# Optimization experiments

Measured on AMD Instinct MI355X. Metric: run time of the kernel, lower is better.

The kernel has to match this reference:

```python
import jax, jax.numpy as jnp
import numpy as np

B, N = 64, 16384
D_WHERE, D_WHAT = 4, 64
MAX_OBJECTS = 512
NEG_PCT = 0.1
NEG_ADDED = int(NEG_PCT * N)          # 1638
K = MAX_OBJECTS + NEG_ADDED           # 2150 objects kept per image (static)
EPS = 1e-3                            # _z_present_eps
PRESENT_THRESH = 0.5                  # deterministic present_fn


def setup_inputs() -> dict:
    key = jax.random.key(0)
    k1, k2, k3, k4, k5, k6 = jax.random.split(key, 6)
    return {
        "z_where": jax.random.normal(k1, (B, N, D_WHERE), dtype=jnp.float32),
        "z_present": jax.random.uniform(k2, (B, N, 1), dtype=jnp.float32),
        "z_what_loc": jax.random.normal(k3, (B, N, D_WHAT), dtype=jnp.float32),
        "z_what_scale": jax.random.uniform(k4, (B, N, D_WHAT), dtype=jnp.float32),
        "z_depth_loc": jax.random.normal(k5, (B, N, 1), dtype=jnp.float32),
        "z_depth_scale": jax.random.uniform(k6, (B, N, 1), dtype=jnp.float32),
    }


def _forward(z_where, z_present, z_what_loc, z_what_scale, z_depth_loc, z_depth_scale):
    # --- reset_non_present ---
    mask = z_present > EPS                                # [B,N,1]
    z_what_loc = jnp.where(mask, z_what_loc, jnp.float32(0.0))
    z_what_scale = jnp.where(mask, z_what_scale, jnp.float32(1.0))
    z_depth_loc = jnp.where(mask, z_depth_loc, jnp.float32(0.0))
    z_depth_scale = jnp.where(mask, z_depth_scale, jnp.float32(1.0))

    # --- sampling fns (deterministic instantiation) ---
    sampled_where = z_where
    sampled_present = (z_present > PRESENT_THRESH).astype(z_present.dtype)  # [B,N,1]
    sampled_what = z_what_loc
    sampled_depth = z_depth_loc

    # --- limit_positive: drop lowest-probability present objects beyond cap ---
    # equivalent to keeping top-MAX_OBJECTS present objects by z_present per row
    p = z_present[..., 0]                                 # [B,N]
    pres = sampled_present[..., 0] > 0                    # [B,N] bool
    score = jnp.where(pres, p, -jnp.inf)
    order = jnp.argsort(-score, axis=1)                   # descending, -inf last
    ranks = jnp.argsort(order, axis=1)                    # rank of each slot
    keep = pres & (ranks < MAX_OBJECTS)                   # [B,N]

    # --- add_negative: mark NEG_ADDED zero slots per row with -1 ---
    # (deterministic stand-in for randperm: take the last NEG_ADDED zero slots)
    zero = ~keep                                          # [B,N]
    zcount = jnp.cumsum(zero.astype(jnp.int32), axis=1)   # [B,N]
    nzeros = zcount[:, -1:]                               # [B,1]
    negative = zero & (zcount > nzeros - NEG_ADDED)
    modified = jnp.where(negative, jnp.float32(-1.0), keep.astype(z_present.dtype))

    # --- filter: gather nonzero slots (exactly K per row) in index order ---
    present_mask = modified != 0                          # [B,N]
    sort_key = jnp.where(present_mask, 0, 1).astype(jnp.int32)
    idx = jnp.argsort(sort_key, axis=1, stable=True)[:, :K]  # [B,K]

    def gather(t):
        return jnp.take_along_axis(t, idx[..., None], axis=1)

    return (
        gather(sampled_where),          # [B,K,4]
        gather(modified[..., None]),    # [B,K,1] values in {-1, 1}
        gather(sampled_what),           # [B,K,64]
        gather(sampled_depth),          # [B,K,1]
    )


def reference(z_where, z_present, z_what_loc, z_what_scale, z_depth_loc, z_depth_scale):
    return _forward(z_where, z_present, z_what_loc, z_what_scale,
                    z_depth_loc, z_depth_scale)
```

## Files before the change

kernel.cpp:

```cpp
#include <hip/hip_runtime.h>
#include <cstdint>

#define NB 64
#define NN 16384
#define DWHERE 4
#define DWHAT 64
#define MAXOBJ 512
#define NEGADD 1638
#define KSEL (MAXOBJ + NEGADD)
#define EPSV 0.001f

__device__ __forceinline__ void scan1024(int* buf, int t) {
  #pragma unroll
  for (int off = 1; off < 1024; off <<= 1) {
    int x = (t >= off) ? buf[t - off] : 0;
    __syncthreads();
    buf[t] += x;
    __syncthreads();
  }
}

__global__ __launch_bounds__(1024) void select_kernel(
    const float* __restrict__ z_present,
    int* __restrict__ ws_idx,
    float* __restrict__ ws_mod)
{
  const int b = blockIdx.x;
  const int t = threadIdx.x;

  __shared__ int hist[4096];
  __shared__ int buf[1024];
  __shared__ int s_B1, s_above1, s_T, s_kTie;

  if (t == 0) { s_B1 = -1; s_above1 = 0; s_T = 0; s_kTie = 0; }

  unsigned int key[16];
  {
    const float4* p4 = (const float4*)(z_present + (size_t)b * NN);
    #pragma unroll
    for (int j = 0; j < 4; ++j) {
      float4 v = p4[t * 4 + j];
      key[4 * j + 0] = (v.x > 0.5f) ? __float_as_uint(v.x) : 0u;
      key[4 * j + 1] = (v.y > 0.5f) ? __float_as_uint(v.y) : 0u;
      key[4 * j + 2] = (v.z > 0.5f) ? __float_as_uint(v.z) : 0u;
      key[4 * j + 3] = (v.w > 0.5f) ? __float_as_uint(v.w) : 0u;
    }
  }

  #pragma unroll
  for (int j = 0; j < 4; ++j) hist[t + 1024 * j] = 0;
  __syncthreads();
  #pragma unroll
  for (int j = 0; j < 16; ++j)
    if (key[j]) atomicAdd(&hist[(key[j] >> 12) - 0x3F000u], 1);
  __syncthreads();

  int h0 = hist[2 * t], h1 = hist[2 * t + 1];
  buf[1023 - t] = h0 + h1;
  __syncthreads();
  scan1024(buf, t);
  int sufP  = buf[1023 - t];
  int sufPn = (t == 1023) ? 0 : buf[1022 - t];
  int presentCount = buf[1023];
  if (presentCount > MAXOBJ) {
    int sufE = sufP;
    int sufO = sufP - h0;
    if (sufE >= MAXOBJ && sufO  < MAXOBJ) { s_B1 = 2 * t;     s_above1 = sufO;  }
    if (sufO >= MAXOBJ && sufPn < MAXOBJ) { s_B1 = 2 * t + 1; s_above1 = sufPn; }
  }
  __syncthreads();

  int B1 = s_B1;
  if (B1 >= 0) {
    unsigned int hi = (unsigned int)B1 + 0x3F000u;
    #pragma unroll
    for (int j = 0; j < 4; ++j) hist[t + 1024 * j] = 0;
    __syncthreads();
    #pragma unroll
    for (int j = 0; j < 16; ++j)
      if (key[j] && ((key[j] >> 12) == hi)) atomicAdd(&hist[key[j] & 0xFFFu], 1);
    __syncthreads();
    int g0 = hist[4 * t], g1 = hist[4 * t + 1], g2 = hist[4 * t + 2], g3 = hist[4 * t + 3];
    buf[1023 - t] = g0 + g1 + g2 + g3;
    __syncthreads();
    scan1024(buf, t);
    int sufQ  = buf[1023 - t];
    int sufQn = (t == 1023) ? 0 : buf[1022 - t];
    int rem = MAXOBJ - s_above1;
    int s0 = sufQ;
    int s1 = s0 - g0;
    int s2 = s1 - g1;
    int s3 = s2 - g2;
    int s4 = sufQn;
    unsigned int baseT = hi << 12;
    if (s0 >= rem && s1 < rem) { s_T = (int)(baseT | (4u * t + 0)); s_kTie = rem - s1; }
    if (s1 >= rem && s2 < rem) { s_T = (int)(baseT | (4u * t + 1)); s_kTie = rem - s2; }
    if (s2 >= rem && s3 < rem) { s_T = (int)(baseT | (4u * t + 2)); s_kTie = rem - s3; }
    if (s3 >= rem && s4 < rem) { s_T = (int)(baseT | (4u * t + 3)); s_kTie = rem - s4; }
  }
  __syncthreads();

  const unsigned int T = (unsigned int)s_T;
  const int kTie = s_kTie;

  int tieCnt = 0;
  if (T) {
    #pragma unroll
    for (int j = 0; j < 16; ++j) tieCnt += (key[j] == T) ? 1 : 0;
  }
  __syncthreads();
  buf[t] = tieCnt;
  __syncthreads();
  scan1024(buf, t);
  int tieBase = buf[t] - tieCnt;

  int keepMask = 0, zc = 0;
  {
    int tr = tieBase;
    #pragma unroll
    for (int j = 0; j < 16; ++j) {
      unsigned int kk = key[j];
      bool kp;
      if (kk > T) kp = true;
      else if (T && kk == T) { kp = (tr < kTie); tr++; }
      else kp = false;
      keepMask |= ((int)kp) << j;
      zc += kp ? 0 : 1;
    }
  }
  __syncthreads();
  buf[t] = zc;
  __syncthreads();
  scan1024(buf, t);
  int zBase = buf[t] - zc;
  int Z = buf[1023];

  int thr = Z - NEGADD; if (thr < 0) thr = 0;
  int keepTotal = NN - Z;
  int KselTot = keepTotal + (Z - thr);
  size_t obase = (size_t)b * KSEL;
  int ze = zBase;
  #pragma unroll
  for (int j = 0; j < 16; ++j) {
    int i = t * 16 + j;
    bool kp = (keepMask >> j) & 1;
    int keepBefore = i - ze;
    int negBefore = ze - thr; if (negBefore < 0) negBefore = 0;
    int selBefore = keepBefore + negBefore;
    if (kp) {
      ws_idx[obase + selBefore] = i;
      ws_mod[obase + selBefore] = 1.0f;
    } else {
      if (ze >= thr) {
        ws_idx[obase + selBefore] = i;
        ws_mod[obase + selBefore] = -1.0f;
      } else if (KselTot < KSEL) {
        int slot2 = KselTot + (i - selBefore);
        if (slot2 < KSEL) { ws_idx[obase + slot2] = i; ws_mod[obase + slot2] = 0.0f; }
      }
      ze++;
    }
  }
}

__global__ __launch_bounds__(256) void gather_kernel(
    const float* __restrict__ z_where,
    const float* __restrict__ z_present,
    const float* __restrict__ z_what,
    const float* __restrict__ z_depth,
    const int* __restrict__ ws_idx,
    const float* __restrict__ ws_mod,
    float* __restrict__ out)
{
  int b = blockIdx.y;
  int tid = blockIdx.x * 256 + threadIdx.x;
  int k = tid >> 4;
  int l = tid & 15;
  if (k >= KSEL) return;
  int r = b * KSEL + k;
  int src = ws_idx[r];
  size_t gsrc = (size_t)b * NN + (unsigned)src;
  float p = z_present[gsrc];
  bool m = p > EPSV;

  float4 v = ((const float4*)(z_what + gsrc * DWHAT))[l];
  if (!m) { v.x = 0.f; v.y = 0.f; v.z = 0.f; v.w = 0.f; }
  float* out2 = out + (size_t)NB * KSEL * (DWHERE + 1);
  ((float4*)(out2 + (size_t)r * DWHAT))[l] = v;

  if (l == 0) {
    ((float4*)out)[r] = ((const float4*)z_where)[gsrc];
    out[(size_t)NB * KSEL * DWHERE + r] = ws_mod[r];
    out[(size_t)NB * KSEL * (DWHERE + 1 + DWHAT) + r] = m ? z_depth[gsrc] : 0.f;
  }
}

extern "C" void kernel_launch(void* const* d_in, const int* in_sizes, int n_in,
                              void* d_out, int out_size, void* d_ws, size_t ws_size,
                              hipStream_t stream) {
  const float* z_where   = (const float*)d_in[0];
  const float* z_present = (const float*)d_in[1];
  const float* z_what    = (const float*)d_in[2];
  const float* z_depth   = (const float*)d_in[4];

  int*   ws_idx = (int*)d_ws;
  float* ws_mod = (float*)((char*)d_ws + (size_t)NB * KSEL * sizeof(int));

  select_kernel<<<NB, 1024, 0, stream>>>(z_present, ws_idx, ws_mod);

  dim3 grid((KSEL * 16 + 255) / 256, NB);
  gather_kernel<<<grid, 256, 0, stream>>>(z_where, z_present, z_what, z_depth,
                                          ws_idx, ws_mod, (float*)d_out);
}
```

Baseline: 449.1 us.

## Use wave-shuffle block scans, merge prefix scans, stash indices in output

Replaces the shared-memory Hillis-Steele scan, which needs about 20 barriers per scan, with a wave-level shuffle scan plus a 16-entry cross-wave sum. The tie-count and keep-count scans are merged into one packed scan by computing the keep count in closed form. Selected indices and the mod values now go straight into the output buffer instead of workspace; the index sits in the first word of each z_what output row until the gather overwrites it. This removes many block barriers and a workspace round-trip. The gather kernel reads the index back from the same row it later overwrites, so correctness depends on each thread group reading before the writes land.

```diff
diff --git a/kernel.cpp b/kernel.cpp
--- a/kernel.cpp
+++ b/kernel.cpp
@@ -10,26 +10,36 @@
 #define KSEL (MAXOBJ + NEGADD)
 #define EPSV 0.001f
 
-__device__ __forceinline__ void scan1024(int* buf, int t) {
-  #pragma unroll
-  for (int off = 1; off < 1024; off <<= 1) {
-    int x = (t >= off) ? buf[t - off] : 0;
-    __syncthreads();
-    buf[t] += x;
-    __syncthreads();
-  }
+__device__ __forceinline__ int scanBlock(int v, int t, int* wsum, int* total) {
+  const int lane = t & 63, wid = t >> 6;
+  #pragma unroll
+  for (int off = 1; off < 64; off <<= 1) {
+    int x = __shfl_up(v, off, 64);
+    if (lane >= off) v += x;
+  }
+  __syncthreads();
+  if (lane == 63) wsum[wid] = v;
+  __syncthreads();
+  int pre = 0, tot = 0;
+  #pragma unroll
+  for (int w = 0; w < 16; ++w) {
+    int s = wsum[w];
+    tot += s;
+    pre += (w < wid) ? s : 0;
+  }
+  *total = tot;
+  return v + pre;
 }
 
 __global__ __launch_bounds__(1024) void select_kernel(
     const float* __restrict__ z_present,
-    int* __restrict__ ws_idx,
-    float* __restrict__ ws_mod)
+    float* __restrict__ out)
 {
   const int b = blockIdx.x;
   const int t = threadIdx.x;
 
   __shared__ int hist[4096];
-  __shared__ int buf[1024];
+  __shared__ int wsum[16];
   __shared__ int s_B1, s_above1, s_T, s_kTie;
 
   if (t == 0) { s_B1 = -1; s_above1 = 0; s_T = 0; s_kTie = 0; }
@@ -55,22 +65,21 @@
     if (key[j]) atomicAdd(&hist[(key[j] >> 12) - 0x3F000u], 1);
   __syncthreads();
 
-  int h0 = hist[2 * t], h1 = hist[2 * t + 1];
-  buf[1023 - t] = h0 + h1;
-  __syncthreads();
-  scan1024(buf, t);
-  int sufP  = buf[1023 - t];
-  int sufPn = (t == 1023) ? 0 : buf[1022 - t];
-  int presentCount = buf[1023];
-  if (presentCount > MAXOBJ) {
-    int sufE = sufP;
-    int sufO = sufP - h0;
-    if (sufE >= MAXOBJ && sufO  < MAXOBJ) { s_B1 = 2 * t;     s_above1 = sufO;  }
-    if (sufO >= MAXOBJ && sufPn < MAXOBJ) { s_B1 = 2 * t + 1; s_above1 = sufPn; }
-  }
-  __syncthreads();
-
-  int B1 = s_B1;
+  {
+    const int q = 1023 - t;
+    int h0 = hist[2 * q], h1 = hist[2 * q + 1];
+    int v = h0 + h1, tot;
+    int s = scanBlock(v, t, wsum, &tot);
+    if (tot > MAXOBJ) {
+      int sufO = s - h0;
+      int sufN = s - v;
+      if (s    >= MAXOBJ && sufO < MAXOBJ) { s_B1 = 2 * q;     s_above1 = sufO; }
+      if (sufO >= MAXOBJ && sufN < MAXOBJ) { s_B1 = 2 * q + 1; s_above1 = sufN; }
+    }
+  }
+  __syncthreads();
+
+  const int B1 = s_B1;
   if (B1 >= 0) {
     unsigned int hi = (unsigned int)B1 + 0x3F000u;
     #pragma unroll
@@ -80,83 +89,77 @@
     for (int j = 0; j < 16; ++j)
       if (key[j] && ((key[j] >> 12) == hi)) atomicAdd(&hist[key[j] & 0xFFFu], 1);
     __syncthreads();
-    int g0 = hist[4 * t], g1 = hist[4 * t + 1], g2 = hist[4 * t + 2], g3 = hist[4 * t + 3];
-    buf[1023 - t] = g0 + g1 + g2 + g3;
-    __syncthreads();
-    scan1024(buf, t);
-    int sufQ  = buf[1023 - t];
-    int sufQn = (t == 1023) ? 0 : buf[1022 - t];
+    const int q = 1023 - t;
+    int g0 = hist[4 * q], g1 = hist[4 * q + 1], g2 = hist[4 * q + 2], g3 = hist[4 * q + 3];
+    int v = g0 + g1 + g2 + g3, tot;
+    int s = scanBlock(v, t, wsum, &tot);
     int rem = MAXOBJ - s_above1;
-    int s0 = sufQ;
+    int s0 = s;
     int s1 = s0 - g0;
     int s2 = s1 - g1;
     int s3 = s2 - g2;
-    int s4 = sufQn;
+    int s4 = s - v;
     unsigned int baseT = hi << 12;
-    if (s0 >= rem && s1 < rem) { s_T = (int)(baseT | (4u * t + 0)); s_kTie = rem - s1; }
-    if (s1 >= rem && s2 < rem) { s_T = (int)(baseT | (4u * t + 1)); s_kTie = rem - s2; }
-    if (s2 >= rem && s3 < rem) { s_T = (int)(baseT | (4u * t + 2)); s_kTie = rem - s3; }
-    if (s3 >= rem && s4 < rem) { s_T = (int)(baseT | (4u * t + 3)); s_kTie = rem - s4; }
+    if (s0 >= rem && s1 < rem) { s_T = (int)(baseT | (4u * q + 0)); s_kTie = rem - s1; }
+    if (s1 >= rem && s2 < rem) { s_T = (int)(baseT | (4u * q + 1)); s_kTie = rem - s2; }
+    if (s2 >= rem && s3 < rem) { s_T = (int)(baseT | (4u * q + 2)); s_kTie = rem - s3; }
+    if (s3 >= rem && s4 < rem) { s_T = (int)(baseT | (4u * q + 3)); s_kTie = rem - s4; }
   }
   __syncthreads();
 
   const unsigned int T = (unsigned int)s_T;
   const int kTie = s_kTie;
 
-  int tieCnt = 0;
-  if (T) {
-    #pragma unroll
-    for (int j = 0; j < 16; ++j) tieCnt += (key[j] == T) ? 1 : 0;
-  }
-  __syncthreads();
-  buf[t] = tieCnt;
-  __syncthreads();
-  scan1024(buf, t);
-  int tieBase = buf[t] - tieCnt;
-
-  int keepMask = 0, zc = 0;
-  {
-    int tr = tieBase;
-    #pragma unroll
-    for (int j = 0; j < 16; ++j) {
-      unsigned int kk = key[j];
-      bool kp;
-      if (kk > T) kp = true;
-      else if (T && kk == T) { kp = (tr < kTie); tr++; }
-      else kp = false;
-      keepMask |= ((int)kp) << j;
-      zc += kp ? 0 : 1;
-    }
-  }
-  __syncthreads();
-  buf[t] = zc;
-  __syncthreads();
-  scan1024(buf, t);
-  int zBase = buf[t] - zc;
-  int Z = buf[1023];
-
+  int a = 0, g = 0;
+  #pragma unroll
+  for (int j = 0; j < 16; ++j) {
+    unsigned int kk = key[j];
+    g += (kk > T) ? 1 : 0;
+    a += (T && kk == T) ? 1 : 0;
+  }
+  int packed = (g << 16) | a, tot;
+  int incl = scanBlock(packed, t, wsum, &tot);
+  int excl = incl - packed;
+  int prefG   = excl >> 16;
+  int tieBase = excl & 0xFFFF;
+  int totG   = tot >> 16;
+  int totTie = tot & 0xFFFF;
+
+  int keepBefore0 = prefG + min(kTie, tieBase);
+  int zBase = 16 * t - keepBefore0;
+  int keepTotal = totG + min(kTie, totTie);
+  int Z = NN - keepTotal;
   int thr = Z - NEGADD; if (thr < 0) thr = 0;
-  int keepTotal = NN - Z;
   int KselTot = keepTotal + (Z - thr);
+
   size_t obase = (size_t)b * KSEL;
-  int ze = zBase;
+  float* out_mod  = out + (size_t)NB * KSEL * DWHERE;
+  float* out_what = out + (size_t)NB * KSEL * (DWHERE + 1);
+  int ze = zBase, tr = tieBase;
   #pragma unroll
   for (int j = 0; j < 16; ++j) {
     int i = t * 16 + j;
-    bool kp = (keepMask >> j) & 1;
+    unsigned int kk = key[j];
+    bool kp;
+    if (kk > T) kp = true;
+    else if (T && kk == T) { kp = (tr < kTie); tr++; }
+    else kp = false;
     int keepBefore = i - ze;
     int negBefore = ze - thr; if (negBefore < 0) negBefore = 0;
     int selBefore = keepBefore + negBefore;
     if (kp) {
-      ws_idx[obase + selBefore] = i;
-      ws_mod[obase + selBefore] = 1.0f;
+      ((int*)out_what)[(obase + (size_t)selBefore) * DWHAT] = i;
+      out_mod[obase + selBefore] = 1.0f;
     } else {
       if (ze >= thr) {
-        ws_idx[obase + selBefore] = i;
-        ws_mod[obase + selBefore] = -1.0f;
+        ((int*)out_what)[(obase + (size_t)selBefore) * DWHAT] = i;
+        out_mod[obase + selBefore] = -1.0f;
       } else if (KselTot < KSEL) {
         int slot2 = KselTot + (i - selBefore);
-        if (slot2 < KSEL) { ws_idx[obase + slot2] = i; ws_mod[obase + slot2] = 0.0f; }
+        if (slot2 < KSEL) {
+          ((int*)out_what)[(obase + (size_t)slot2) * DWHAT] = i;
+          out_mod[obase + slot2] = 0.0f;
+        }
       }
       ze++;
     }
@@ -168,8 +171,6 @@
     const float* __restrict__ z_present,
     const float* __restrict__ z_what,
     const float* __restrict__ z_depth,
-    const int* __restrict__ ws_idx,
-    const float* __restrict__ ws_mod,
     float* __restrict__ out)
 {
   int b = blockIdx.y;
@@ -177,20 +178,19 @@
   int k = tid >> 4;
   int l = tid & 15;
   if (k >= KSEL) return;
-  int r = b * KSEL + k;
-  int src = ws_idx[r];
+  size_t r = (size_t)b * KSEL + k;
+  float* out_what = out + (size_t)NB * KSEL * (DWHERE + 1);
+  int src = ((const int*)out_what)[r * DWHAT] & (NN - 1);
   size_t gsrc = (size_t)b * NN + (unsigned)src;
   float p = z_present[gsrc];
   bool m = p > EPSV;
 
   float4 v = ((const float4*)(z_what + gsrc * DWHAT))[l];
   if (!m) { v.x = 0.f; v.y = 0.f; v.z = 0.f; v.w = 0.f; }
-  float* out2 = out + (size_t)NB * KSEL * (DWHERE + 1);
-  ((float4*)(out2 + (size_t)r * DWHAT))[l] = v;
+  ((float4*)(out_what + r * DWHAT))[l] = v;
 
   if (l == 0) {
     ((float4*)out)[r] = ((const float4*)z_where)[gsrc];
-    out[(size_t)NB * KSEL * DWHERE + r] = ws_mod[r];
     out[(size_t)NB * KSEL * (DWHERE + 1 + DWHAT) + r] = m ? z_depth[gsrc] : 0.f;
   }
 }
@@ -203,12 +203,11 @@
   const float* z_what    = (const float*)d_in[2];
   const float* z_depth   = (const float*)d_in[4];
 
-  int*   ws_idx = (int*)d_ws;
-  float* ws_mod = (float*)((char*)d_ws + (size_t)NB * KSEL * sizeof(int));
-
-  select_kernel<<<NB, 1024, 0, stream>>>(z_present, ws_idx, ws_mod);
+  (void)d_ws; (void)ws_size;
+
+  select_kernel<<<NB, 1024, 0, stream>>>(z_present, (float*)d_out);
 
   dim3 grid((KSEL * 16 + 255) / 256, NB);
   gather_kernel<<<grid, 256, 0, stream>>>(z_where, z_present, z_what, z_depth,
-                                          ws_idx, ws_mod, (float*)d_out);
-}
+                                          (float*)d_out);
+}
```

Measured after the change: 453.5 us. No clear change (+1.0%).
